# Kernel tuning notes

Hardware: AMD Instinct MI355X
Metric: run time of the kernel (lower is better)

The kernel has to match this reference:

```python
import jax, jax.numpy as jnp
import numpy as np

T, B, H, R = 4096, 32, 512, 512

def setup_inputs() -> dict:
    key = jax.random.key(0)
    k1, k2, k3, k4 = jax.random.split(key, 4)
    return {
        "encoded_contribution": jax.random.normal(k1, (T, B, H), dtype=jnp.float32),
        "mask": jnp.zeros((T, B), dtype=jnp.float32),
        "rnn_state": jax.random.normal(k2, (B, R), dtype=jnp.float32),
        "prev_att_weights": jnp.zeros((T, B), dtype=jnp.float32),
        "W_rec": jax.random.normal(k3, (H, R), dtype=jnp.float32) * 0.05,
        "w_score": jax.random.normal(k4, (H,), dtype=jnp.float32) * 0.05,
        "b_score": jnp.zeros((1,), dtype=jnp.float32),
    }

def reference(encoded_contribution, mask, rnn_state, prev_att_weights, W_rec, w_score, b_score):
    # rec_state_to_hidden (no bias): (B,R) @ (R,H) -> (B,H), broadcast over T
    rec = jnp.einsum('br,hr->bh', rnn_state, W_rec)
    hidden = encoded_contribution + rec[None, :, :]          # (T,B,H)
    # hidden_to_score: H -> 1, squeeze
    scores = jnp.einsum('tbh,h->tb', jnp.tanh(hidden), w_score) + b_score[0]
    scores = scores + mask                                    # additive mask (-1e5 for pad)
    att_weights = jax.nn.softmax(scores, axis=0)              # softmax over time T
    return att_weights
```

## Files before the change

kernel.cpp:

```cpp
#include <hip/hip_runtime.h>
#include <math.h>

__device__ __forceinline__ float wave_reduce_sum(float v) {
    #pragma unroll
    for (int off = 32; off > 0; off >>= 1)
        v += __shfl_xor(v, off, 64);
    return v;
}

__global__ void rec_kernel(const float* __restrict__ rnn,
                           const float* __restrict__ Wrec,
                           float* __restrict__ rec,
                           int B, int H, int R) {
    int w    = (blockIdx.x * blockDim.x + threadIdx.x) >> 6;
    int lane = threadIdx.x & 63;
    int nOut = B * H;
    if (w >= nOut) return;
    int b = w / H;
    int h = w - b * H;
    const float* xr = rnn  + (size_t)b * R;
    const float* wr = Wrec + (size_t)h * R;
    float acc = 0.f;
    for (int r = lane * 4; r < R; r += 256) {
        float4 a = *(const float4*)(xr + r);
        float4 c = *(const float4*)(wr + r);
        acc += a.x * c.x + a.y * c.y + a.z * c.z + a.w * c.w;
    }
    acc = wave_reduce_sum(acc);
    if (lane == 0) rec[w] = acc;
}

__device__ __forceinline__ float fast_tanh(float x) {
    float e = __expf(2.0f * x);
    return 1.0f - 2.0f * __builtin_amdgcn_rcpf(e + 1.0f);
}

__global__ void score_kernel(const float* __restrict__ enc,
                             const float* __restrict__ mask,
                             const float* __restrict__ rec,
                             const float* __restrict__ wsc,
                             const float* __restrict__ bsc,
                             float* __restrict__ scores,
                             int TB, int B, int H) {
    int w    = (blockIdx.x * blockDim.x + threadIdx.x) >> 6;
    int lane = threadIdx.x & 63;
    if (w >= TB) return;
    int b = w % B;
    const float* er = enc + (size_t)w * H;
    const float* rr = rec + (size_t)b * H;
    float acc = 0.f;
    for (int h = lane * 4; h < H; h += 256) {
        float4 e  = *(const float4*)(er + h);
        float4 rv = *(const float4*)(rr + h);
        float4 wv = *(const float4*)(wsc + h);
        acc += wv.x * fast_tanh(e.x + rv.x);
        acc += wv.y * fast_tanh(e.y + rv.y);
        acc += wv.z * fast_tanh(e.z + rv.z);
        acc += wv.w * fast_tanh(e.w + rv.w);
    }
    acc = wave_reduce_sum(acc);
    if (lane == 0) scores[w] = acc + bsc[0] + mask[w];
}

__global__ void softmax_kernel(float* __restrict__ out, int T, int B) {
    const int b   = blockIdx.x;
    const int tid = threadIdx.x;
    const int nth = blockDim.x;

    float sv[32];
    int   n = 0;
    float m = -INFINITY;
    for (int t = tid; t < T; t += nth) {
        float s = out[(size_t)t * B + b];
        sv[n++] = s;
        m = fmaxf(m, s);
    }

    __shared__ float red[8];
    const int wid  = tid >> 6;
    const int lane = tid & 63;
    const int nw   = nth >> 6;

    #pragma unroll
    for (int off = 32; off > 0; off >>= 1)
        m = fmaxf(m, __shfl_xor(m, off, 64));
    if (lane == 0) red[wid] = m;
    __syncthreads();
    if (tid == 0) {
        float mm = red[0];
        for (int i = 1; i < nw; i++) mm = fmaxf(mm, red[i]);
        red[0] = mm;
    }
    __syncthreads();
    m = red[0];

    float sum = 0.f;
    for (int i = 0; i < n; i++) {
        sv[i] = __expf(sv[i] - m);
        sum += sv[i];
    }
    sum = wave_reduce_sum(sum);
    __syncthreads();
    if (lane == 0) red[wid] = sum;
    __syncthreads();
    if (tid == 0) {
        float ss = red[0];
        for (int i = 1; i < nw; i++) ss += red[i];
        red[0] = ss;
    }
    __syncthreads();
    float inv = 1.0f / red[0];

    n = 0;
    for (int t = tid; t < T; t += nth) {
        out[(size_t)t * B + b] = sv[n++] * inv;
    }
}

extern "C" void kernel_launch(void* const* d_in, const int* in_sizes, int n_in,
                              void* d_out, int out_size, void* d_ws, size_t ws_size,
                              hipStream_t stream) {
    const float* enc  = (const float*)d_in[0];
    const float* mask = (const float*)d_in[1];
    const float* rnn  = (const float*)d_in[2];
    const float* Wrec = (const float*)d_in[4];
    const float* wsc  = (const float*)d_in[5];
    const float* bsc  = (const float*)d_in[6];

    const int H = in_sizes[5];
    const int R = in_sizes[4] / H;
    const int B = in_sizes[2] / R;
    const int T = in_sizes[1] / B;
    const int TB = T * B;

    float* rec    = (float*)d_ws;
    float* scores = (float*)d_out;

    {
        int nOut   = B * H;
        int blocks = (nOut + 3) / 4;
        rec_kernel<<<blocks, 256, 0, stream>>>(rnn, Wrec, rec, B, H, R);
    }
    {
        int blocks = (TB + 3) / 4;
        score_kernel<<<blocks, 256, 0, stream>>>(enc, mask, rec, wsc, bsc,
                                                 scores, TB, B, H);
    }
    softmax_kernel<<<B, 256, 0, stream>>>(scores, T, B);
}
```

Before: 63.86 us.

## Process multiple time rows per wave and write transposed scores for softmax

The score kernel now has each wave handle 16 consecutive time steps for one batch index. The rec and w_score vectors are loaded once per wave instead of once per row, and the wave processes two halves of H per row. Scores are written to a workspace in (B,T) layout, so the softmax kernel can read them with contiguous float4 loads using T/4 threads per block, and its block reductions now use a wave shuffle. The kernel now hard-codes H=512, T divisible by 16, and T/4 threads per block (1024). Softmax output stores are still strided by B, and the score writes are scattered by T.

```diff
diff --git a/kernel.cpp b/kernel.cpp
--- a/kernel.cpp
+++ b/kernel.cpp
@@ -6,6 +6,17 @@
     for (int off = 32; off > 0; off >>= 1)
         v += __shfl_xor(v, off, 64);
     return v;
+}
+__device__ __forceinline__ float wave_reduce_max(float v) {
+    #pragma unroll
+    for (int off = 32; off > 0; off >>= 1)
+        v = fmaxf(v, __shfl_xor(v, off, 64));
+    return v;
+}
+
+__device__ __forceinline__ float fast_tanh(float x) {
+    float e = __expf(2.0f * x);
+    return 1.0f - 2.0f * __builtin_amdgcn_rcpf(e + 1.0f);
 }
 
 __global__ void rec_kernel(const float* __restrict__ rnn,
@@ -30,91 +41,101 @@
     if (lane == 0) rec[w] = acc;
 }
 
-__device__ __forceinline__ float fast_tanh(float x) {
-    float e = __expf(2.0f * x);
-    return 1.0f - 2.0f * __builtin_amdgcn_rcpf(e + 1.0f);
-}
-
+#define SCORE_ROWS 16
 __global__ void score_kernel(const float* __restrict__ enc,
                              const float* __restrict__ mask,
                              const float* __restrict__ rec,
                              const float* __restrict__ wsc,
                              const float* __restrict__ bsc,
-                             float* __restrict__ scores,
-                             int TB, int B, int H) {
-    int w    = (blockIdx.x * blockDim.x + threadIdx.x) >> 6;
-    int lane = threadIdx.x & 63;
-    if (w >= TB) return;
-    int b = w % B;
-    const float* er = enc + (size_t)w * H;
+                             float* __restrict__ scores_t,
+                             int T, int B, int H) {
+    const int w    = (blockIdx.x * blockDim.x + threadIdx.x) >> 6;
+    const int lane = threadIdx.x & 63;
+    const int b     = w % B;
+    const int tbase = (w / B) * SCORE_ROWS;
+    if (tbase >= T) return;
+
+    const int h0 = lane * 4;
+    const int h1 = (H >> 1) + h0;
+
     const float* rr = rec + (size_t)b * H;
-    float acc = 0.f;
-    for (int h = lane * 4; h < H; h += 256) {
-        float4 e  = *(const float4*)(er + h);
-        float4 rv = *(const float4*)(rr + h);
-        float4 wv = *(const float4*)(wsc + h);
-        acc += wv.x * fast_tanh(e.x + rv.x);
-        acc += wv.y * fast_tanh(e.y + rv.y);
-        acc += wv.z * fast_tanh(e.z + rv.z);
-        acc += wv.w * fast_tanh(e.w + rv.w);
+    float4 r0 = *(const float4*)(rr + h0);
+    float4 r1 = *(const float4*)(rr + h1);
+    float4 w0 = *(const float4*)(wsc + h0);
+    float4 w1 = *(const float4*)(wsc + h1);
+    const float bias = bsc[0];
+
+    const float* erow = enc + ((size_t)tbase * B + b) * H;
+    const size_t rstride = (size_t)B * H;
+
+    #pragma unroll
+    for (int i = 0; i < SCORE_ROWS; ++i) {
+        const float* er = erow + (size_t)i * rstride;
+        float4 e0 = *(const float4*)(er + h0);
+        float4 e1 = *(const float4*)(er + h1);
+        float acc;
+        acc  = w0.x * fast_tanh(e0.x + r0.x);
+        acc += w0.y * fast_tanh(e0.y + r0.y);
+        acc += w0.z * fast_tanh(e0.z + r0.z);
+        acc += w0.w * fast_tanh(e0.w + r0.w);
+        acc += w1.x * fast_tanh(e1.x + r1.x);
+        acc += w1.y * fast_tanh(e1.y + r1.y);
+        acc += w1.z * fast_tanh(e1.z + r1.z);
+        acc += w1.w * fast_tanh(e1.w + r1.w);
+        acc = wave_reduce_sum(acc);
+        if (lane == 0) {
+            const int t = tbase + i;
+            scores_t[(size_t)b * T + t] = acc + bias + mask[(size_t)t * B + b];
+        }
     }
-    acc = wave_reduce_sum(acc);
-    if (lane == 0) scores[w] = acc + bsc[0] + mask[w];
 }
 
-__global__ void softmax_kernel(float* __restrict__ out, int T, int B) {
-    const int b   = blockIdx.x;
-    const int tid = threadIdx.x;
-    const int nth = blockDim.x;
-
-    float sv[32];
-    int   n = 0;
-    float m = -INFINITY;
-    for (int t = tid; t < T; t += nth) {
-        float s = out[(size_t)t * B + b];
-        sv[n++] = s;
-        m = fmaxf(m, s);
-    }
-
-    __shared__ float red[8];
+__global__ void softmax_kernel(const float* __restrict__ scores_t,
+                               float* __restrict__ out, int T, int B) {
+    const int b    = blockIdx.x;
+    const int tid  = threadIdx.x;
     const int wid  = tid >> 6;
     const int lane = tid & 63;
-    const int nw   = nth >> 6;
+    const int nw   = blockDim.x >> 6;
 
-    #pragma unroll
-    for (int off = 32; off > 0; off >>= 1)
-        m = fmaxf(m, __shfl_xor(m, off, 64));
+    float4 v = *(const float4*)(scores_t + (size_t)b * T + tid * 4);
+
+    __shared__ float red[16];
+
+    float m = fmaxf(fmaxf(v.x, v.y), fmaxf(v.z, v.w));
+    m = wave_reduce_max(m);
     if (lane == 0) red[wid] = m;
     __syncthreads();
-    if (tid == 0) {
-        float mm = red[0];
-        for (int i = 1; i < nw; i++) mm = fmaxf(mm, red[i]);
-        red[0] = mm;
+    if (tid < 64) {
+        float mm = (tid < nw) ? red[tid] : -INFINITY;
+        mm = wave_reduce_max(mm);
+        if (tid == 0) red[0] = mm;
     }
     __syncthreads();
     m = red[0];
+    __syncthreads();
 
-    float sum = 0.f;
-    for (int i = 0; i < n; i++) {
-        sv[i] = __expf(sv[i] - m);
-        sum += sv[i];
-    }
-    sum = wave_reduce_sum(sum);
+    v.x = __expf(v.x - m);
+    v.y = __expf(v.y - m);
+    v.z = __expf(v.z - m);
+    v.w = __expf(v.w - m);
+    float s = (v.x + v.y) + (v.z + v.w);
+    s = wave_reduce_sum(s);
+    if (lane == 0) red[wid] = s;
     __syncthreads();
-    if (lane == 0) red[wid] = sum;
-    __syncthreads();
-    if (tid == 0) {
-        float ss = red[0];
-        for (int i = 1; i < nw; i++) ss += red[i];
-        red[0] = ss;
+    if (tid < 64) {
+        float ss = (tid < nw) ? red[tid] : 0.f;
+        ss = wave_reduce_sum(ss);
+        if (tid == 0) red[0] = ss;
     }
     __syncthreads();
-    float inv = 1.0f / red[0];
+    const float inv = 1.0f / red[0];
 
-    n = 0;
-    for (int t = tid; t < T; t += nth) {
-        out[(size_t)t * B + b] = sv[n++] * inv;
-    }
+    const int t0 = tid * 4;
+    out[(size_t)(t0 + 0) * B + b] = v.x * inv;
+    out[(size_t)(t0 + 1) * B + b] = v.y * inv;
+    out[(size_t)(t0 + 2) * B + b] = v.z * inv;
+    out[(size_t)(t0 + 3) * B + b] = v.w * inv;
 }
 
 extern "C" void kernel_launch(void* const* d_in, const int* in_sizes, int n_in,
@@ -131,10 +152,10 @@
     const int R = in_sizes[4] / H;
     const int B = in_sizes[2] / R;
     const int T = in_sizes[1] / B;
-    const int TB = T * B;
 
-    float* rec    = (float*)d_ws;
-    float* scores = (float*)d_out;
+    float* rec      = (float*)d_ws;
+    float* scores_t = (float*)d_ws + (size_t)B * H;
+    float* out      = (float*)d_out;
 
     {
         int nOut   = B * H;
@@ -142,9 +163,10 @@
         rec_kernel<<<blocks, 256, 0, stream>>>(rnn, Wrec, rec, B, H, R);
     }
     {
-        int blocks = (TB + 3) / 4;
+        int nWaves = (T / SCORE_ROWS) * B;
+        int blocks = (nWaves + 3) / 4;
         score_kernel<<<blocks, 256, 0, stream>>>(enc, mask, rec, wsc, bsc,
-                                                 scores, TB, B, H);
+                                                 scores_t, T, B, H);
     }
-    softmax_kernel<<<B, 256, 0, stream>>>(scores, T, B);
+    softmax_kernel<<<B, T / 4, 0, stream>>>(scores_t, out, T, B);
 }
```

New measurement: 56.07 us. 1.14x faster.

## Fuse partial softmax stats into score kernel and parallelize finalize over time

Applied to the files above, without the earlier changes.

The score kernel now processes chunks of time steps per block. Each wave handles four batch rows and keeps rec and w_score in registers. The kernel also computes per-chunk max and sum-of-exp partials, writing them and the raw scores to workspace. A new finalize kernel merges the partials and normalizes across many blocks, replacing the 32-block serial softmax. This targets the poorly parallel softmax pass and the repeated reloads of rec and w_score, at the cost of extra workspace traffic and a hardcoded layout assuming B=32 and H=512.

```diff
diff --git a/kernel.cpp b/kernel.cpp
--- a/kernel.cpp
+++ b/kernel.cpp
@@ -1,11 +1,20 @@
 #include <hip/hip_runtime.h>
 #include <math.h>
+
+typedef float vf4 __attribute__((ext_vector_type(4)));
+
+#define T_CHUNK 8
 
 __device__ __forceinline__ float wave_reduce_sum(float v) {
     #pragma unroll
     for (int off = 32; off > 0; off >>= 1)
         v += __shfl_xor(v, off, 64);
     return v;
+}
+
+__device__ __forceinline__ float fast_tanh(float x) {
+    float e = __expf(2.0f * x);
+    return 1.0f - 2.0f * __builtin_amdgcn_rcpf(e + 1.0f);
 }
 
 __global__ void rec_kernel(const float* __restrict__ rnn,
@@ -22,17 +31,12 @@
     const float* wr = Wrec + (size_t)h * R;
     float acc = 0.f;
     for (int r = lane * 4; r < R; r += 256) {
-        float4 a = *(const float4*)(xr + r);
-        float4 c = *(const float4*)(wr + r);
+        vf4 a = *(const vf4*)(xr + r);
+        vf4 c = *(const vf4*)(wr + r);
         acc += a.x * c.x + a.y * c.y + a.z * c.z + a.w * c.w;
     }
     acc = wave_reduce_sum(acc);
     if (lane == 0) rec[w] = acc;
-}
-
-__device__ __forceinline__ float fast_tanh(float x) {
-    float e = __expf(2.0f * x);
-    return 1.0f - 2.0f * __builtin_amdgcn_rcpf(e + 1.0f);
 }
 
 __global__ void score_kernel(const float* __restrict__ enc,
@@ -41,79 +45,126 @@
                              const float* __restrict__ wsc,
                              const float* __restrict__ bsc,
                              float* __restrict__ scores,
-                             int TB, int B, int H) {
-    int w    = (blockIdx.x * blockDim.x + threadIdx.x) >> 6;
-    int lane = threadIdx.x & 63;
-    if (w >= TB) return;
-    int b = w % B;
-    const float* er = enc + (size_t)w * H;
-    const float* rr = rec + (size_t)b * H;
-    float acc = 0.f;
-    for (int h = lane * 4; h < H; h += 256) {
-        float4 e  = *(const float4*)(er + h);
-        float4 rv = *(const float4*)(rr + h);
-        float4 wv = *(const float4*)(wsc + h);
-        acc += wv.x * fast_tanh(e.x + rv.x);
-        acc += wv.y * fast_tanh(e.y + rv.y);
-        acc += wv.z * fast_tanh(e.z + rv.z);
-        acc += wv.w * fast_tanh(e.w + rv.w);
-    }
-    acc = wave_reduce_sum(acc);
-    if (lane == 0) scores[w] = acc + bsc[0] + mask[w];
-}
-
-__global__ void softmax_kernel(float* __restrict__ out, int T, int B) {
-    const int b   = blockIdx.x;
+                             float* __restrict__ pm,
+                             float* __restrict__ ps,
+                             int T, int B, int H) {
+    const int tid  = threadIdx.x;
+    const int wi   = tid >> 6;
+    const int lane = tid & 63;
+    const int t0   = blockIdx.x * T_CHUNK;
+    const int b0   = wi * 4;
+
+    __shared__ float sc_lds[T_CHUNK][32];
+
+    vf4 w0 = *(const vf4*)(wsc + lane * 4);
+    vf4 w1 = *(const vf4*)(wsc + 256 + lane * 4);
+    vf4 rr[8];
+    #pragma unroll
+    for (int j = 0; j < 8; ++j)
+        rr[j] = *(const vf4*)(rec + (size_t)(b0 + (j >> 1)) * H
+                                   + ((j & 1) << 8) + lane * 4);
+    const float bias = bsc[0];
+
+    for (int ti = 0; ti < T_CHUNK; ++ti) {
+        const float* rowp = enc + ((size_t)(t0 + ti) * B + b0) * H;
+        float a[4] = {0.f, 0.f, 0.f, 0.f};
+        #pragma unroll
+        for (int j = 0; j < 8; ++j) {
+            vf4 e  = *(const vf4*)(rowp + j * 256 + lane * 4);
+            vf4 rv = rr[j];
+            vf4 wv = (j & 1) ? w1 : w0;
+            float p;
+            p  = wv.x * fast_tanh(e.x + rv.x);
+            p += wv.y * fast_tanh(e.y + rv.y);
+            p += wv.z * fast_tanh(e.z + rv.z);
+            p += wv.w * fast_tanh(e.w + rv.w);
+            a[j >> 1] += p;
+        }
+        #pragma unroll
+        for (int s = 0; s < 2; ++s) {
+            const int bit = 1 << s;
+            #pragma unroll
+            for (int i = 0; i < (4 >> (s + 1)); ++i) {
+                float sent = (lane & bit) ? a[2 * i]     : a[2 * i + 1];
+                float keep = (lane & bit) ? a[2 * i + 1] : a[2 * i];
+                a[i] = keep + __shfl_xor(sent, bit, 64);
+            }
+        }
+        a[0] += __shfl_xor(a[0], 4, 64);
+        a[0] += __shfl_xor(a[0], 8, 64);
+        a[0] += __shfl_xor(a[0], 16, 64);
+        a[0] += __shfl_xor(a[0], 32, 64);
+        if (lane < 4) sc_lds[ti][b0 + lane] = a[0] + bias;
+    }
+    __syncthreads();
+
+    if (tid < T_CHUNK * 32) {
+        const int tl = tid >> 5, b = tid & 31;
+        float v = sc_lds[tl][b] + mask[(size_t)(t0 + tl) * B + b];
+        scores[(size_t)(t0 + tl) * B + b] = v;
+        sc_lds[tl][b] = v;
+    }
+    __syncthreads();
+
+    if (tid < 32) {
+        float m = -INFINITY;
+        #pragma unroll
+        for (int tl = 0; tl < T_CHUNK; ++tl)
+            m = fmaxf(m, sc_lds[tl][tid]);
+        float s = 0.f;
+        #pragma unroll
+        for (int tl = 0; tl < T_CHUNK; ++tl)
+            s += __expf(sc_lds[tl][tid] - m);
+        pm[(size_t)blockIdx.x * 32 + tid] = m;
+        ps[(size_t)blockIdx.x * 32 + tid] = s;
+    }
+}
+
+__global__ void finalize_kernel(const float* __restrict__ scores,
+                                const float* __restrict__ pm,
+                                const float* __restrict__ ps,
+                                float* __restrict__ out,
+                                int T, int B, int NCH) {
+    __shared__ float red[8][32];
+    __shared__ float Ml[32], Sl[32];
     const int tid = threadIdx.x;
-    const int nth = blockDim.x;
-
-    float sv[32];
-    int   n = 0;
+    const int b   = tid & 31;
+    const int sl  = tid >> 5;
+    const int cps = NCH / 8;
+
     float m = -INFINITY;
-    for (int t = tid; t < T; t += nth) {
-        float s = out[(size_t)t * B + b];
-        sv[n++] = s;
-        m = fmaxf(m, s);
-    }
-
-    __shared__ float red[8];
-    const int wid  = tid >> 6;
-    const int lane = tid & 63;
-    const int nw   = nth >> 6;
-
+    for (int c = sl * cps; c < (sl + 1) * cps; ++c)
+        m = fmaxf(m, pm[(size_t)c * 32 + b]);
+    red[sl][b] = m;
+    __syncthreads();
+    if (tid < 32) {
+        float M = -INFINITY;
+        #pragma unroll
+        for (int s = 0; s < 8; ++s) M = fmaxf(M, red[s][tid]);
+        Ml[tid] = M;
+    }
+    __syncthreads();
+    const float M = Ml[b];
+    float s = 0.f;
+    for (int c = sl * cps; c < (sl + 1) * cps; ++c)
+        s += ps[(size_t)c * 32 + b] * __expf(pm[(size_t)c * 32 + b] - M);
+    red[sl][b] = s;
+    __syncthreads();
+    if (tid < 32) {
+        float S = 0.f;
+        #pragma unroll
+        for (int s2 = 0; s2 < 8; ++s2) S += red[s2][tid];
+        Sl[tid] = 1.0f / S;
+    }
+    __syncthreads();
+    const float Sinv = Sl[b];
+
+    const int t0 = blockIdx.x * 64;
     #pragma unroll
-    for (int off = 32; off > 0; off >>= 1)
-        m = fmaxf(m, __shfl_xor(m, off, 64));
-    if (lane == 0) red[wid] = m;
-    __syncthreads();
-    if (tid == 0) {
-        float mm = red[0];
-        for (int i = 1; i < nw; i++) mm = fmaxf(mm, red[i]);
-        red[0] = mm;
-    }
-    __syncthreads();
-    m = red[0];
-
-    float sum = 0.f;
-    for (int i = 0; i < n; i++) {
-        sv[i] = __expf(sv[i] - m);
-        sum += sv[i];
-    }
-    sum = wave_reduce_sum(sum);
-    __syncthreads();
-    if (lane == 0) red[wid] = sum;
-    __syncthreads();
-    if (tid == 0) {
-        float ss = red[0];
-        for (int i = 1; i < nw; i++) ss += red[i];
-        red[0] = ss;
-    }
-    __syncthreads();
-    float inv = 1.0f / red[0];
-
-    n = 0;
-    for (int t = tid; t < T; t += nth) {
-        out[(size_t)t * B + b] = sv[n++] * inv;
+    for (int i = 0; i < 8; ++i) {
+        int t = t0 + i * 8 + sl;
+        float x = scores[(size_t)t * B + b];
+        out[(size_t)t * B + b] = __expf(x - M) * Sinv;
     }
 }
 
@@ -131,20 +182,20 @@
     const int R = in_sizes[4] / H;
     const int B = in_sizes[2] / R;
     const int T = in_sizes[1] / B;
-    const int TB = T * B;
+    const int NCH = T / T_CHUNK;
 
     float* rec    = (float*)d_ws;
-    float* scores = (float*)d_out;
+    float* scores = rec + (size_t)B * H;
+    float* pm     = scores + (size_t)T * B;
+    float* ps     = pm + (size_t)NCH * B;
+    float* out    = (float*)d_out;
 
     {
         int nOut   = B * H;
         int blocks = (nOut + 3) / 4;
         rec_kernel<<<blocks, 256, 0, stream>>>(rnn, Wrec, rec, B, H, R);
     }
-    {
-        int blocks = (TB + 3) / 4;
-        score_kernel<<<blocks, 256, 0, stream>>>(enc, mask, rec, wsc, bsc,
-                                                 scores, TB, B, H);
-    }
-    softmax_kernel<<<B, 256, 0, stream>>>(scores, T, B);
-}
+    score_kernel<<<NCH, 512, 0, stream>>>(enc, mask, rec, wsc, bsc,
+                                          scores, pm, ps, T, B, H);
+    finalize_kernel<<<T / 64, 256, 0, stream>>>(scores, pm, ps, out, T, B, NCH);
+}
```

Measured after the change: 84.09 us. +31.7%, slower.
